# Optimization experiments

Hardware: AMD Instinct MI355X
Metric: run time of the kernel (lower is better)

Reference implementation:

```python
import jax, jax.numpy as jnp
import numpy as np

NU, NI, D, E = 100000, 50000, 128, 500000


def setup_inputs() -> dict:
    key = jax.random.key(0)
    ks = jax.random.split(key, 10)
    s = 1.0 / np.sqrt(D)
    return {
        "feat_user": jax.random.normal(ks[0], (NU, D), jnp.float32),
        "feat_item": jax.random.normal(ks[1], (NI, D), jnp.float32),
        "W1": jax.random.normal(ks[2], (D, D), jnp.float32) * s,
        "b1": jnp.zeros((D,), jnp.float32),
        "W2": jax.random.normal(ks[3], (D, D), jnp.float32) * s,
        "b2": jnp.zeros((D,), jnp.float32),
        "norm_u2i": jax.random.uniform(ks[4], (E, 1), jnp.float32),
        "norm_i2u": jax.random.uniform(ks[5], (E, 1), jnp.float32),
        "edge_u2i_src": jax.random.randint(ks[6], (E,), 0, NU, jnp.int32),
        "edge_u2i_dst": jax.random.randint(ks[7], (E,), 0, NI, jnp.int32),
        "edge_i2u_src": jax.random.randint(ks[8], (E,), 0, NI, jnp.int32),
        "edge_i2u_dst": jax.random.randint(ks[9], (E,), 0, NU, jnp.int32),
    }


def reference(feat_user, feat_item, W1, b1, W2, b2, norm_u2i, norm_i2u,
              edge_u2i_src, edge_u2i_dst, edge_i2u_src, edge_i2u_dst):
    lin1 = lambda x: x @ W1 + b1
    lin2 = lambda x: x @ W2 + b2

    # self-loop etypes: copy_u(W1(feat)) summed over one self-edge per node
    h_user = lin1(feat_user)
    h_item = lin1(feat_item)

    # user -> item edges: norm * (W1(e_u) + W2(e_u * e_i)), scatter-sum to items
    su = feat_user[edge_u2i_src]            # [E, D]
    di = feat_item[edge_u2i_dst]            # [E, D]
    m_ui = norm_u2i * (lin1(su) + lin2(su * di))
    h_item = h_item + jax.ops.segment_sum(m_ui, edge_u2i_dst, num_segments=feat_item.shape[0])

    # item -> user edges
    si = feat_item[edge_i2u_src]
    du = feat_user[edge_i2u_dst]
    m_iu = norm_i2u * (lin1(si) + lin2(si * du))
    h_user = h_user + jax.ops.segment_sum(m_iu, edge_i2u_dst, num_segments=feat_user.shape[0])

    def finish(h):
        h = jax.nn.leaky_relu(h, 0.2)       # LeakyReLU(0.2); dropout p=0 is identity
        n = jnp.linalg.norm(h, axis=1, keepdims=True)
        return h / jnp.maximum(n, 1e-12)    # F.normalize(dim=1, p=2), eps=1e-12

    return finish(h_user), finish(h_item)
```

## Files before the change

### kernel.cpp

```cpp
#include <hip/hip_runtime.h>

#define DD 128
#define SCAN_TILE 1024
#define HS 136
#define FR 16

typedef __attribute__((ext_vector_type(8))) short short8;
typedef __attribute__((ext_vector_type(4))) float f32x4;
typedef __attribute__((ext_vector_type(2))) float f32x2;

__device__ inline unsigned short f2bf_rne(float f) {
    unsigned int u = __float_as_uint(f);
    unsigned int r = u + 0x7FFFu + ((u >> 16) & 1u);
    return (unsigned short)(r >> 16);
}
__device__ inline float bf2f(unsigned short h) {
    return __uint_as_float(((unsigned int)h) << 16);
}
__device__ inline void split2(float a, float b, unsigned int& hi, unsigned int& lo) {
    unsigned short ha = f2bf_rne(a), hb = f2bf_rne(b);
    float la = a - bf2f(ha), lb = b - bf2f(hb);
    hi = (unsigned int)ha | ((unsigned int)hb << 16);
    lo = (unsigned int)f2bf_rne(la) | ((unsigned int)f2bf_rne(lb) << 16);
}

__global__ __launch_bounds__(256) void count_wprep_kernel(
    const int* __restrict__ dst1, int E1, int* deg1,
    const int* __restrict__ dst2, int E2, int* deg2,
    const float* __restrict__ W1, const float* __restrict__ W2,
    unsigned short* wfrag)
{
    int b = blockIdx.x;
    if (b < 16) {
        int t = b * 256 + threadIdx.x;
        int lane = t & 63;
        int cf   = (t >> 6) & 7;
        int ksm  = (t >> 9) & 3;
        int mat  = t >> 11;
        const float* W = mat ? W2 : W1;
        int g = lane >> 4, c = lane & 15;
        int n = cf * 16 + c;
        unsigned int hi[4], lo[4];
        #pragma unroll
        for (int p = 0; p < 4; ++p) {
            int k0 = ksm * 32 + g * 8 + p * 2;
            float v0 = W[(size_t)k0 * DD + n];
            float v1 = W[(size_t)(k0 + 1) * DD + n];
            split2(v0, v1, hi[p], lo[p]);
        }
        unsigned short* dh = wfrag + (size_t)mat * 32768
                           + ((size_t)(ksm * 8 + cf) * 64 + lane) * 8;
        unsigned short* dl = dh + 16384;
        *(uint4*)dh = make_uint4(hi[0], hi[1], hi[2], hi[3]);
        *(uint4*)dl = make_uint4(lo[0], lo[1], lo[2], lo[3]);
        return;
    }
    int t = (b - 16) * 256 + threadIdx.x;
    if (t < E1) {
        atomicAdd(deg1 + dst1[t], 1);
    } else if (t - E1 < E2) {
        atomicAdd(deg2 + dst2[t - E1], 1);
    }
}

__global__ __launch_bounds__(256) void scanA_kernel(
    const int* __restrict__ cur_i, int NI,
    const int* __restrict__ cur_u, int NU,
    int* bsum, int nb0)
{
    int b = blockIdx.x;
    const int* cur;
    int N, base;
    if (b < nb0) { cur = cur_i; N = NI; base = b * SCAN_TILE; }
    else         { cur = cur_u; N = NU; base = (b - nb0) * SCAN_TILE; }
    int t = threadIdx.x;
    int idx0 = base + t * 4;
    int s = 0;
    #pragma unroll
    for (int k = 0; k < 4; ++k) {
        int idx = idx0 + k;
        if (idx < N) s += cur[idx];
    }
    __shared__ int red[256];
    red[t] = s;
    __syncthreads();
    for (int o = 128; o >= 1; o >>= 1) {
        if (t < o) red[t] += red[t + o];
        __syncthreads();
    }
    if (t == 0) bsum[b] = red[0];
}

__global__ __launch_bounds__(256) void scanC_kernel(
    int* cur_i, int* row_i, int NI,
    int* cur_u, int* row_u, int NU,
    const int* __restrict__ bsum, int nb0, int nb1)
{
    __shared__ int bs[512];
    __shared__ int ps[256];
    __shared__ int sh[256];
    int b = blockIdx.x;
    int t = threadIdx.x;
    int ntot = nb0 + nb1;

    bs[t]       = (t < ntot)       ? bsum[t]       : 0;
    bs[256 + t] = (256 + t < ntot) ? bsum[256 + t] : 0;
    __syncthreads();
    int b0v = bs[2 * t], b1v = bs[2 * t + 1];
    int pair = b0v + b1v;
    ps[t] = pair;
    __syncthreads();
    for (int o = 1; o < 256; o <<= 1) {
        int u = (t >= o) ? ps[t - o] : 0;
        __syncthreads();
        ps[t] += u;
        __syncthreads();
    }
    int e0 = ps[t] - pair;
    __syncthreads();
    bs[2 * t]     = e0;
    bs[2 * t + 1] = e0 + b0v;
    __syncthreads();
    int grand = ps[255];
    int totI  = bs[nb0];
    if (b == 0 && t == 0) {
        row_i[NI] = totI;
        row_u[NU] = grand - totI;
    }
    int off = (b < nb0) ? bs[b] : bs[b] - totI;

    int* cur; int* row;
    int N, base;
    if (b < nb0) { cur = cur_i; row = row_i; N = NI; base = b * SCAN_TILE; }
    else         { cur = cur_u; row = row_u; N = NU; base = (b - nb0) * SCAN_TILE; }
    int idx0 = base + t * 4;
    int v[4];
    int s = 0;
    #pragma unroll
    for (int k = 0; k < 4; ++k) {
        int idx = idx0 + k;
        v[k] = (idx < N) ? cur[idx] : 0;
        s += v[k];
    }
    sh[t] = s;
    __syncthreads();
    for (int o = 1; o < 256; o <<= 1) {
        int u = (t >= o) ? sh[t - o] : 0;
        __syncthreads();
        sh[t] += u;
        __syncthreads();
    }
    int run = off + sh[t] - s;
    #pragma unroll
    for (int k = 0; k < 4; ++k) {
        int idx = idx0 + k;
        if (idx < N) {
            row[idx] = run;
            cur[idx] = run;
            run += v[k];
        }
    }
}

__global__ __launch_bounds__(256) void fill_pg_kernel(
    const int* __restrict__ dst1, const int* __restrict__ src1,
    const float* __restrict__ norm1, int E1, int* cur1, int2* esn1,
    const int* __restrict__ dst2, const int* __restrict__ src2,
    const float* __restrict__ norm2, int E2, int* cur2, int2* esn2)
{
    int t = blockIdx.x * 256 + threadIdx.x;
    if (t < E1) {
        int pos = atomicAdd(cur1 + dst1[t], 1);
        esn1[pos] = make_int2(src1[t], __float_as_int(norm1[t]));
    } else if (t - E1 < E2) {
        int e = t - E1;
        int pos = atomicAdd(cur2 + dst2[e], 1);
        esn2[pos] = make_int2(src2[e], __float_as_int(norm2[e]));
    }
}


__global__ __launch_bounds__(256) void scatter_kernel(
    const float* __restrict__ feat_src,
    const int* __restrict__ src,
    const int* __restrict__ dst,
    const float* __restrict__ norm,
    float* agg,
    float* ssum,
    int E)
{
    int gw = (int)((blockIdx.x * 256u + threadIdx.x) >> 6);
    int lane = threadIdx.x & 63;
    if (gw >= E) return;
    int si = src[gw];
    int di = dst[gw];
    float nv = norm[gw];
    float2 v = *(const float2*)(feat_src + (size_t)si * DD + lane * 2);
    float* ap = agg + (size_t)di * DD + lane * 2;
    unsafeAtomicAdd(ap,     v.x * nv);
    unsafeAtomicAdd(ap + 1, v.y * nv);
    if (lane == 0) unsafeAtomicAdd(ssum + di, nv);
}

__global__ __launch_bounds__(256, 8) void fused_kernel(
    const float* __restrict__ feat_user, const float* __restrict__ feat_item,
    const int* __restrict__ row_u, const int2* __restrict__ esnU,
    int NU, int nbU,
    const int* __restrict__ row_i, const int2* __restrict__ esnI, int NI,
    const unsigned short* __restrict__ wfrag,
    const float* __restrict__ b1, const float* __restrict__ b2,
    float* out_base)
{
    __shared__ __align__(16) char smem[FR * 512 * 2];
    __shared__ float sst[FR];

    const float *featO, *featS;
    const int *row;
    const int2 *esn;
    float* out;
    int row0, nrows;
    if ((int)blockIdx.x < nbU) {
        featO = feat_user; featS = feat_item; row = row_u; esn = esnU;
        out = out_base; row0 = blockIdx.x * FR; nrows = NU;
    } else {
        featO = feat_item; featS = feat_user; row = row_i; esn = esnI;
        out = out_base + (size_t)NU * DD;
        row0 = (blockIdx.x - nbU) * FR; nrows = NI;
    }

    int t = threadIdx.x;
    int w = t >> 6;
    int lane = t & 63;
    char* pAh = smem;
    char* pAl = smem + FR * 512;

    for (int rr = 0; rr < 4; ++rr) {
        int r = w * 4 + rr;
        int grow = row0 + r;
        float2 acc = {0.f, 0.f};
        float sn = 0.f;
        f32x2 f2 = {0.f, 0.f};
        if (grow < nrows) {
            f2 = __builtin_nontemporal_load(
                     (const f32x2*)(featO + (size_t)grow * DD + lane * 2));
            int beg = row[grow], end = row[grow + 1];
            int j = beg;
            for (; j + 6 <= end; j += 6) {
                int2 e0 = esn[j],     e1 = esn[j + 1], e2 = esn[j + 2];
                int2 e3 = esn[j + 3], e4 = esn[j + 4], e5 = esn[j + 5];
                const float* fb = featS + lane * 2;
                float2 v0 = *(const float2*)(fb + ((size_t)e0.x << 7));
                float2 v1 = *(const float2*)(fb + ((size_t)e1.x << 7));
                float2 v2 = *(const float2*)(fb + ((size_t)e2.x << 7));
                float2 v3 = *(const float2*)(fb + ((size_t)e3.x << 7));
                float2 v4 = *(const float2*)(fb + ((size_t)e4.x << 7));
                float2 v5 = *(const float2*)(fb + ((size_t)e5.x << 7));
                float n0 = __int_as_float(e0.y), n1 = __int_as_float(e1.y);
                float n2 = __int_as_float(e2.y), n3 = __int_as_float(e3.y);
                float n4 = __int_as_float(e4.y), n5 = __int_as_float(e5.y);
                acc.x += n0 * v0.x + n1 * v1.x + n2 * v2.x
                       + n3 * v3.x + n4 * v4.x + n5 * v5.x;
                acc.y += n0 * v0.y + n1 * v1.y + n2 * v2.y
                       + n3 * v3.y + n4 * v4.y + n5 * v5.y;
                sn += n0 + n1 + n2 + n3 + n4 + n5;
            }
            for (; j + 2 <= end; j += 2) {
                int2 e0 = esn[j], e1 = esn[j + 1];
                const float* fb = featS + lane * 2;
                float2 v0 = *(const float2*)(fb + ((size_t)e0.x << 7));
                float2 v1 = *(const float2*)(fb + ((size_t)e1.x << 7));
                float n0 = __int_as_float(e0.y), n1 = __int_as_float(e1.y);
                acc.x += n0 * v0.x + n1 * v1.x;
                acc.y += n0 * v0.y + n1 * v1.y;
                sn += n0 + n1;
            }
            if (j < end) {
                int2 e0 = esn[j];
                float n0 = __int_as_float(e0.y);
                float2 v0 = *(const float2*)(featS + ((size_t)e0.x << 7) + lane * 2);
                acc.x += n0 * v0.x;
                acc.y += n0 * v0.y;
                sn += n0;
            }
        }
        float x0 = f2.x + acc.x, x1 = f2.y + acc.y;
        float y0 = f2.x * acc.x, y1 = f2.y * acc.y;
        unsigned int xh, xl, yh, yl;
        split2(x0, x1, xh, xl);
        split2(y0, y1, yh, yl);
        int swz = (r & 7) << 4;
        int rb = r * 512;
        int xo = rb + ((4 * lane) ^ swz);
        int yo = rb + ((256 + 4 * lane) ^ swz);
        *(unsigned int*)(pAh + xo) = xh;
        *(unsigned int*)(pAl + xo) = xl;
        *(unsigned int*)(pAh + yo) = yh;
        *(unsigned int*)(pAl + yo) = yl;
        if (lane == 0) sst[r] = sn;
    }
    __syncthreads();

    int r16 = lane & 15, g = lane >> 4;
    f32x4 acc0 = {0.f,0.f,0.f,0.f}, acc1 = {0.f,0.f,0.f,0.f};
    const char* cAh = (const char*)pAh;
    const char* cAl = (const char*)pAl;
    int swzA = (r16 & 7) << 4;
    int ob0 = r16 * 512;

    #pragma unroll 2
    for (int ks = 0; ks < 8; ++ks) {
        int offx = (ks * 64 + g * 16) ^ swzA;
        short8 a0h = *(const short8*)(cAh + ob0 + offx);
        short8 a0l = *(const short8*)(cAl + ob0 + offx);
        int mat = ks >> 2, ksm = ks & 3;
        const unsigned short* ph = wfrag + (size_t)mat * 32768;
        const unsigned short* pl = ph + 16384;
        int bo0 = ((ksm * 8 + w * 2) * 64 + lane) * 8;
        int bo1 = bo0 + 512;
        short8 b0h = *(const short8*)(ph + bo0);
        short8 b0l = *(const short8*)(pl + bo0);
        short8 b1h = *(const short8*)(ph + bo1);
        short8 b1l = *(const short8*)(pl + bo1);
        acc0 = __builtin_amdgcn_mfma_f32_16x16x32_bf16(a0h, b0h, acc0, 0, 0, 0);
        acc0 = __builtin_amdgcn_mfma_f32_16x16x32_bf16(a0h, b0l, acc0, 0, 0, 0);
        acc0 = __builtin_amdgcn_mfma_f32_16x16x32_bf16(a0l, b0h, acc0, 0, 0, 0);
        acc1 = __builtin_amdgcn_mfma_f32_16x16x32_bf16(a0h, b1h, acc1, 0, 0, 0);
        acc1 = __builtin_amdgcn_mfma_f32_16x16x32_bf16(a0h, b1l, acc1, 0, 0, 0);
        acc1 = __builtin_amdgcn_mfma_f32_16x16x32_bf16(a0l, b1h, acc1, 0, 0, 0);
    }
    __syncthreads();

    float* hbuf = (float*)smem;
    #pragma unroll
    for (int j = 0; j < 4; ++j) {
        int rA = g * 4 + j;
        hbuf[rA * HS + (w * 32 + r16)]      = acc0[j];
        hbuf[rA * HS + (w * 32 + 16 + r16)] = acc1[j];
    }
    __syncthreads();

    int c0 = t & 63, c1 = c0 + 64, rg = t >> 6;
    float b1c0 = b1[c0], b1c1 = b1[c1];
    float b2c0 = b2[c0], b2c1 = b2[c1];
    #pragma unroll
    for (int rr = 0; rr < 4; ++rr) {
        int lr = rg * 4 + rr;
        int row_ = row0 + lr;
        if (row_ < nrows) {
            float s = sst[lr];
            float h0 = hbuf[lr * HS + c0] + (1.0f + s) * b1c0 + s * b2c0;
            float h1 = hbuf[lr * HS + c1] + (1.0f + s) * b1c1 + s * b2c1;
            h0 = h0 >= 0.f ? h0 : 0.2f * h0;
            h1 = h1 >= 0.f ? h1 : 0.2f * h1;
            float loc = h0 * h0 + h1 * h1;
            #pragma unroll
            for (int m = 32; m >= 1; m >>= 1) loc += __shfl_xor(loc, m, 64);
            float inv = 1.0f / fmaxf(sqrtf(loc), 1e-12f);
            __builtin_nontemporal_store(h0 * inv, out + (size_t)row_ * DD + c0);
            __builtin_nontemporal_store(h1 * inv, out + (size_t)row_ * DD + c1);
        }
    }
}


__global__ __launch_bounds__(256) void finish_kernel(
    const float* __restrict__ feat,
    const float* agg,
    const float* __restrict__ ssum,
    const float* __restrict__ W1,
    const float* __restrict__ b1,
    const float* __restrict__ W2,
    const float* __restrict__ b2,
    float* out,
    int nrows)
{
    __shared__ float xs[32][DD];
    __shared__ float ys[32][DD];
    int row0 = blockIdx.x * 32;
    int tid = threadIdx.x;

    for (int i = tid; i < 32 * (DD / 4); i += 256) {
        int r = i >> 5;
        int c4 = (i & 31) * 4;
        int row = row0 + r;
        if (row < nrows) {
            float4 f = *(const float4*)(feat + (size_t)row * DD + c4);
            float4 a = *(const float4*)(agg  + (size_t)row * DD + c4);
            float4 x, y;
            x.x = f.x + a.x; x.y = f.y + a.y; x.z = f.z + a.z; x.w = f.w + a.w;
            y.x = f.x * a.x; y.y = f.y * a.y; y.z = f.z * a.z; y.w = f.w * a.w;
            *(float4*)&xs[r][c4] = x;
            *(float4*)&ys[r][c4] = y;
        }
    }
    __syncthreads();

    int c0 = tid & 63;
    int rg = tid >> 6;
    int c1 = c0 + 64;

    float acc[8][2] = {{0.f,0.f},{0.f,0.f},{0.f,0.f},{0.f,0.f},
                       {0.f,0.f},{0.f,0.f},{0.f,0.f},{0.f,0.f}};
    for (int k = 0; k < DD; k += 4) {
        float w1a[4], w1b[4], w2a[4], w2b[4];
        #pragma unroll
        for (int kk = 0; kk < 4; ++kk) {
            const float* wr1 = W1 + (size_t)(k + kk) * DD;
            const float* wr2 = W2 + (size_t)(k + kk) * DD;
            w1a[kk] = wr1[c0]; w1b[kk] = wr1[c1];
            w2a[kk] = wr2[c0]; w2b[kk] = wr2[c1];
        }
        #pragma unroll
        for (int r = 0; r < 8; ++r) {
            float4 xv = *(const float4*)&xs[rg * 8 + r][k];
            float4 yv = *(const float4*)&ys[rg * 8 + r][k];
            acc[r][0] += xv.x*w1a[0] + xv.y*w1a[1] + xv.z*w1a[2] + xv.w*w1a[3]
                       + yv.x*w2a[0] + yv.y*w2a[1] + yv.z*w2a[2] + yv.w*w2a[3];
            acc[r][1] += xv.x*w1b[0] + xv.y*w1b[1] + xv.z*w1b[2] + xv.w*w1b[3]
                       + yv.x*w2b[0] + yv.y*w2b[1] + yv.z*w2b[2] + yv.w*w2b[3];
        }
    }

    float b1c0 = b1[c0], b1c1 = b1[c1];
    float b2c0 = b2[c0], b2c1 = b2[c1];

    #pragma unroll
    for (int r = 0; r < 8; ++r) {
        int row = row0 + rg * 8 + r;
        if (row < nrows) {
            float s = ssum[row];
            float h0 = acc[r][0] + (1.0f + s) * b1c0 + s * b2c0;
            float h1 = acc[r][1] + (1.0f + s) * b1c1 + s * b2c1;
            h0 = h0 >= 0.f ? h0 : 0.2f * h0;
            h1 = h1 >= 0.f ? h1 : 0.2f * h1;
            float loc = h0 * h0 + h1 * h1;
            #pragma unroll
            for (int m = 32; m >= 1; m >>= 1) loc += __shfl_xor(loc, m, 64);
            float inv = 1.0f / fmaxf(sqrtf(loc), 1e-12f);
            out[(size_t)row * DD + c0] = h0 * inv;
            out[(size_t)row * DD + c1] = h1 * inv;
        }
    }
}

extern "C" void kernel_launch(void* const* d_in, const int* in_sizes, int n_in,
                              void* d_out, int out_size, void* d_ws, size_t ws_size,
                              hipStream_t stream) {
    const float* feat_user = (const float*)d_in[0];
    const float* feat_item = (const float*)d_in[1];
    const float* W1        = (const float*)d_in[2];
    const float* b1        = (const float*)d_in[3];
    const float* W2        = (const float*)d_in[4];
    const float* b2        = (const float*)d_in[5];
    const float* norm_u2i  = (const float*)d_in[6];
    const float* norm_i2u  = (const float*)d_in[7];
    const int* eus = (const int*)d_in[8];
    const int* eud = (const int*)d_in[9];
    const int* eis = (const int*)d_in[10];
    const int* eid = (const int*)d_in[11];

    int NU = in_sizes[0] / DD;
    int NI = in_sizes[1] / DD;
    int E1 = in_sizes[8];
    int E2 = in_sizes[10];
    float* out = (float*)d_out;

    int nb0 = (NI + SCAN_TILE - 1) / SCAN_TILE;
    int nb1 = (NU + SCAN_TILE - 1) / SCAN_TILE;
    int nbU = (NU + FR - 1) / FR;
    int nbI = (NI + FR - 1) / FR;

    size_t wfrag_bytes = 131072;
    size_t need_pg   = wfrag_bytes + 64  +
                       ((size_t)3 * NU + 3 * NI + 2 * E1 + 2 * E2 + 2
                        + nb0 + nb1) * sizeof(int);

    int eb = (int)(((long long)E1 + E2 + 255) / 256);

    if (ws_size >= need_pg && nb0 + nb1 <= 512) {
        unsigned short* wfrag = (unsigned short*)d_ws;
        int* cur_i = (int*)((char*)d_ws + wfrag_bytes);
        int* cur_u = cur_i + NI;
        int* row_i = cur_u + NU;
        int* row_u = row_i + NI + 1;
        int* pend  = row_u + NU + 1;
        int2* esn1 = (int2*)(((uintptr_t)pend + 15) & ~(uintptr_t)15);
        int2* esn2 = esn1 + E1;
        int* bsum  = (int*)(esn2 + E2);

        hipMemsetAsync(cur_i, 0, (size_t)(NI + NU) * sizeof(int), stream);

        count_wprep_kernel<<<16 + eb, 256, 0, stream>>>(
            eud, E1, cur_i, eid, E2, cur_u, W1, W2, wfrag);
        scanA_kernel<<<nb0 + nb1, 256, 0, stream>>>(cur_i, NI, cur_u, NU,
                                                    bsum, nb0);
        scanC_kernel<<<nb0 + nb1, 256, 0, stream>>>(cur_i, row_i, NI,
                                                    cur_u, row_u, NU,
                                                    bsum, nb0, nb1);
        fill_pg_kernel<<<eb, 256, 0, stream>>>(
            eud, eus, norm_u2i, E1, cur_i, esn1,
            eid, eis, norm_i2u, E2, cur_u, esn2);

        fused_kernel<<<nbU + nbI, 256, 0, stream>>>(
            feat_user, feat_item,
            row_u, esn2, NU, nbU,
            row_i, esn1, NI,
            wfrag, b1, b2, out);
    } else {
        float* agg_user = out;
        float* agg_item = out + (size_t)NU * DD;
        float* s_user = (float*)d_ws;
        float* s_item = s_user + NU;

        hipMemsetAsync(out, 0, (size_t)out_size * sizeof(float), stream);
        hipMemsetAsync(d_ws, 0, (size_t)(NU + NI) * sizeof(float), stream);

        int b1n = (int)(((long long)E1 * 64 + 255) / 256);
        scatter_kernel<<<b1n, 256, 0, stream>>>(feat_user, eus, eud, norm_u2i,
                                                agg_item, s_item, E1);
        int b2n = (int)(((long long)E2 * 64 + 255) / 256);
        scatter_kernel<<<b2n, 256, 0, stream>>>(feat_item, eis, eid, norm_i2u,
                                                agg_user, s_user, E2);

        finish_kernel<<<(NU + 31) / 32, 256, 0, stream>>>(
            feat_user, agg_user, s_user, W1, b1, W2, b2, out, NU);
        finish_kernel<<<(NI + 31) / 32, 256, 0, stream>>>(
            feat_item, agg_item, s_item, W1, b1, W2, b2,
            out + (size_t)NU * DD, NI);
    }
}
```

Measured before the change: 374.1 us.

## Merge CSR build stages into one cooperative kernel with grid syncs

Replaces the memset plus four separate preprocessing kernels (degree count with weight prep, two scan passes, edge fill) with a single cooperative kernel of 1024 blocks that separates the phases with grid.sync. The goal is to remove per-launch overhead and the gaps between dependent launches. In exchange the edge loops become grid-stride over a fixed grid, and each grid barrier costs time. The cooperative launch also requires all blocks to be co-resident, or it fails.

```diff
diff --git a/kernel.cpp b/kernel.cpp
--- a/kernel.cpp
+++ b/kernel.cpp
@@ -1,9 +1,13 @@
 #include <hip/hip_runtime.h>
+#include <hip/hip_cooperative_groups.h>
+
+namespace cg = cooperative_groups;
 
 #define DD 128
 #define SCAN_TILE 1024
 #define HS 136
 #define FR 16
+#define PREP_GRID 1024
 
 typedef __attribute__((ext_vector_type(8))) short short8;
 typedef __attribute__((ext_vector_type(4))) float f32x4;
@@ -24,19 +28,36 @@
     lo = (unsigned int)f2bf_rne(la) | ((unsigned int)f2bf_rne(lb) << 16);
 }
 
-__global__ __launch_bounds__(256) void count_wprep_kernel(
-    const int* __restrict__ dst1, int E1, int* deg1,
-    const int* __restrict__ dst2, int E2, int* deg2,
+__global__ __launch_bounds__(256, 4) void prep_kernel(
+    const int* __restrict__ eud, const int* __restrict__ eus,
+    const float* __restrict__ norm1, int E1,
+    const int* __restrict__ eid, const int* __restrict__ eis,
+    const float* __restrict__ norm2, int E2,
+    int* cur_i, int* cur_u, int* row_i, int* row_u,
+    int2* esn1, int2* esn2, int* bsum,
+    int nb0, int nb1, int NI, int NU,
     const float* __restrict__ W1, const float* __restrict__ W2,
     unsigned short* wfrag)
 {
-    int b = blockIdx.x;
+    cg::grid_group grid = cg::this_grid();
+    __shared__ int red[256];
+    __shared__ int bs[512];
+    __shared__ int ps[256];
+    __shared__ int sh[256];
+
+    int b   = blockIdx.x;
+    int t   = threadIdx.x;
+    int nB  = gridDim.x;
+    int gid = b * 256 + t;
+    int gsz = nB * 256;
+
+    for (int i = gid; i < NI + NU; i += gsz) cur_i[i] = 0;
     if (b < 16) {
-        int t = b * 256 + threadIdx.x;
-        int lane = t & 63;
-        int cf   = (t >> 6) & 7;
-        int ksm  = (t >> 9) & 3;
-        int mat  = t >> 11;
+        int tt = b * 256 + t;
+        int lane = tt & 63;
+        int cf   = (tt >> 6) & 7;
+        int ksm  = (tt >> 9) & 3;
+        int mat  = tt >> 11;
         const float* W = mat ? W2 : W1;
         int g = lane >> 4, c = lane & 15;
         int n = cf * 16 + c;
@@ -53,58 +74,40 @@
         unsigned short* dl = dh + 16384;
         *(uint4*)dh = make_uint4(hi[0], hi[1], hi[2], hi[3]);
         *(uint4*)dl = make_uint4(lo[0], lo[1], lo[2], lo[3]);
-        return;
-    }
-    int t = (b - 16) * 256 + threadIdx.x;
-    if (t < E1) {
-        atomicAdd(deg1 + dst1[t], 1);
-    } else if (t - E1 < E2) {
-        atomicAdd(deg2 + dst2[t - E1], 1);
-    }
-}
-
-__global__ __launch_bounds__(256) void scanA_kernel(
-    const int* __restrict__ cur_i, int NI,
-    const int* __restrict__ cur_u, int NU,
-    int* bsum, int nb0)
-{
-    int b = blockIdx.x;
-    const int* cur;
-    int N, base;
-    if (b < nb0) { cur = cur_i; N = NI; base = b * SCAN_TILE; }
-    else         { cur = cur_u; N = NU; base = (b - nb0) * SCAN_TILE; }
-    int t = threadIdx.x;
-    int idx0 = base + t * 4;
-    int s = 0;
-    #pragma unroll
-    for (int k = 0; k < 4; ++k) {
-        int idx = idx0 + k;
-        if (idx < N) s += cur[idx];
-    }
-    __shared__ int red[256];
-    red[t] = s;
-    __syncthreads();
-    for (int o = 128; o >= 1; o >>= 1) {
-        if (t < o) red[t] += red[t + o];
+    }
+    grid.sync();
+
+    for (int i = gid; i < E1 + E2; i += gsz) {
+        if (i < E1) atomicAdd(cur_i + eud[i], 1);
+        else        atomicAdd(cur_u + eid[i - E1], 1);
+    }
+    grid.sync();
+
+    int ntiles = nb0 + nb1;
+    for (int tile = b; tile < ntiles; tile += nB) {
+        const int* cur; int N, base;
+        if (tile < nb0) { cur = cur_i; N = NI; base = tile * SCAN_TILE; }
+        else            { cur = cur_u; N = NU; base = (tile - nb0) * SCAN_TILE; }
+        int idx0 = base + t * 4;
+        int s = 0;
+        #pragma unroll
+        for (int k = 0; k < 4; ++k) {
+            int idx = idx0 + k;
+            if (idx < N) s += cur[idx];
+        }
+        red[t] = s;
         __syncthreads();
-    }
-    if (t == 0) bsum[b] = red[0];
-}
-
-__global__ __launch_bounds__(256) void scanC_kernel(
-    int* cur_i, int* row_i, int NI,
-    int* cur_u, int* row_u, int NU,
-    const int* __restrict__ bsum, int nb0, int nb1)
-{
-    __shared__ int bs[512];
-    __shared__ int ps[256];
-    __shared__ int sh[256];
-    int b = blockIdx.x;
-    int t = threadIdx.x;
-    int ntot = nb0 + nb1;
-
-    bs[t]       = (t < ntot)       ? bsum[t]       : 0;
-    bs[256 + t] = (256 + t < ntot) ? bsum[256 + t] : 0;
+        for (int o = 128; o >= 1; o >>= 1) {
+            if (t < o) red[t] += red[t + o];
+            __syncthreads();
+        }
+        if (t == 0) bsum[tile] = red[0];
+        __syncthreads();
+    }
+    grid.sync();
+
+    bs[t]       = (t < ntiles)       ? bsum[t]       : 0;
+    bs[256 + t] = (256 + t < ntiles) ? bsum[256 + t] : 0;
     __syncthreads();
     int b0v = bs[2 * t], b1v = bs[2 * t + 1];
     int pair = b0v + b1v;
@@ -127,55 +130,52 @@
         row_i[NI] = totI;
         row_u[NU] = grand - totI;
     }
-    int off = (b < nb0) ? bs[b] : bs[b] - totI;
-
-    int* cur; int* row;
-    int N, base;
-    if (b < nb0) { cur = cur_i; row = row_i; N = NI; base = b * SCAN_TILE; }
-    else         { cur = cur_u; row = row_u; N = NU; base = (b - nb0) * SCAN_TILE; }
-    int idx0 = base + t * 4;
-    int v[4];
-    int s = 0;
-    #pragma unroll
-    for (int k = 0; k < 4; ++k) {
-        int idx = idx0 + k;
-        v[k] = (idx < N) ? cur[idx] : 0;
-        s += v[k];
-    }
-    sh[t] = s;
-    __syncthreads();
-    for (int o = 1; o < 256; o <<= 1) {
-        int u = (t >= o) ? sh[t - o] : 0;
+    for (int tile = b; tile < ntiles; tile += nB) {
+        int off = (tile < nb0) ? bs[tile] : bs[tile] - totI;
+        int* cur; int* row;
+        int N, base;
+        if (tile < nb0) { cur = cur_i; row = row_i; N = NI; base = tile * SCAN_TILE; }
+        else            { cur = cur_u; row = row_u; N = NU; base = (tile - nb0) * SCAN_TILE; }
+        int idx0 = base + t * 4;
+        int v[4];
+        int s = 0;
+        #pragma unroll
+        for (int k = 0; k < 4; ++k) {
+            int idx = idx0 + k;
+            v[k] = (idx < N) ? cur[idx] : 0;
+            s += v[k];
+        }
+        sh[t] = s;
         __syncthreads();
-        sh[t] += u;
+        for (int o = 1; o < 256; o <<= 1) {
+            int u = (t >= o) ? sh[t - o] : 0;
+            __syncthreads();
+            sh[t] += u;
+            __syncthreads();
+        }
+        int run = off + sh[t] - s;
+        #pragma unroll
+        for (int k = 0; k < 4; ++k) {
+            int idx = idx0 + k;
+            if (idx < N) {
+                row[idx] = run;
+                cur[idx] = run;
+                run += v[k];
+            }
+        }
         __syncthreads();
     }
-    int run = off + sh[t] - s;
-    #pragma unroll
-    for (int k = 0; k < 4; ++k) {
-        int idx = idx0 + k;
-        if (idx < N) {
-            row[idx] = run;
-            cur[idx] = run;
-            run += v[k];
-        }
-    }
-}
-
-__global__ __launch_bounds__(256) void fill_pg_kernel(
-    const int* __restrict__ dst1, const int* __restrict__ src1,
-    const float* __restrict__ norm1, int E1, int* cur1, int2* esn1,
-    const int* __restrict__ dst2, const int* __restrict__ src2,
-    const float* __restrict__ norm2, int E2, int* cur2, int2* esn2)
-{
-    int t = blockIdx.x * 256 + threadIdx.x;
-    if (t < E1) {
-        int pos = atomicAdd(cur1 + dst1[t], 1);
-        esn1[pos] = make_int2(src1[t], __float_as_int(norm1[t]));
-    } else if (t - E1 < E2) {
-        int e = t - E1;
-        int pos = atomicAdd(cur2 + dst2[e], 1);
-        esn2[pos] = make_int2(src2[e], __float_as_int(norm2[e]));
+    grid.sync();
+
+    for (int i = gid; i < E1 + E2; i += gsz) {
+        if (i < E1) {
+            int pos = atomicAdd(cur_i + eud[i], 1);
+            esn1[pos] = make_int2(eus[i], __float_as_int(norm1[i]));
+        } else {
+            int e = i - E1;
+            int pos = atomicAdd(cur_u + eid[e], 1);
+            esn2[pos] = make_int2(eis[e], __float_as_int(norm2[e]));
+        }
     }
 }
 
@@ -475,8 +475,6 @@
                        ((size_t)3 * NU + 3 * NI + 2 * E1 + 2 * E2 + 2
                         + nb0 + nb1) * sizeof(int);
 
-    int eb = (int)(((long long)E1 + E2 + 255) / 256);
-
     if (ws_size >= need_pg && nb0 + nb1 <= 512) {
         unsigned short* wfrag = (unsigned short*)d_ws;
         int* cur_i = (int*)((char*)d_ws + wfrag_bytes);
@@ -488,18 +486,17 @@
         int2* esn2 = esn1 + E1;
         int* bsum  = (int*)(esn2 + E2);
 
-        hipMemsetAsync(cur_i, 0, (size_t)(NI + NU) * sizeof(int), stream);
-
-        count_wprep_kernel<<<16 + eb, 256, 0, stream>>>(
-            eud, E1, cur_i, eid, E2, cur_u, W1, W2, wfrag);
-        scanA_kernel<<<nb0 + nb1, 256, 0, stream>>>(cur_i, NI, cur_u, NU,
-                                                    bsum, nb0);
-        scanC_kernel<<<nb0 + nb1, 256, 0, stream>>>(cur_i, row_i, NI,
-                                                    cur_u, row_u, NU,
-                                                    bsum, nb0, nb1);
-        fill_pg_kernel<<<eb, 256, 0, stream>>>(
-            eud, eus, norm_u2i, E1, cur_i, esn1,
-            eid, eis, norm_i2u, E2, cur_u, esn2);
+        void* args[] = {
+            (void*)&eud, (void*)&eus, (void*)&norm_u2i, (void*)&E1,
+            (void*)&eid, (void*)&eis, (void*)&norm_i2u, (void*)&E2,
+            (void*)&cur_i, (void*)&cur_u, (void*)&row_i, (void*)&row_u,
+            (void*)&esn1, (void*)&esn2, (void*)&bsum,
+            (void*)&nb0, (void*)&nb1, (void*)&NI, (void*)&NU,
+            (void*)&W1, (void*)&W2, (void*)&wfrag
+        };
+        hipLaunchCooperativeKernel((void*)prep_kernel,
+                                   dim3(PREP_GRID), dim3(256),
+                                   args, 0, stream);
 
         fused_kernel<<<nbU + nbI, 256, 0, stream>>>(
             feat_user, feat_item,
```

Measured after the change: 829.6 us. 122% more time.
